# Optimization experiments

Measured on AMD Instinct MI355X. Metric: run time of the kernel, lower is better.

Reference implementation:

```python
import jax, jax.numpy as jnp
import numpy as np

N_HEADS = 12


def _sink_window_visible(S, num_sink_tokens, window_size):
    # visible[i, j] = (j <= i) and (j < num_sink or j >= i - window + 1)
    i = jnp.arange(S)[:, None]
    j = jnp.arange(S)[None, :]
    return (j <= i) & ((j < num_sink_tokens) | (j >= i - window_size + 1))


def setup_inputs() -> dict:
    key = jax.random.key(0)
    k1, k2, k3 = jax.random.split(key, 3)
    B, S, D = 1, 4096, 768
    hidden_states = jax.random.normal(k1, (B, S, D), dtype=jnp.float32)
    w_attn = jax.random.normal(k2, (D, 3 * D), dtype=jnp.float32) * 0.02
    b_attn = jnp.zeros((3 * D,), dtype=jnp.float32)
    w_proj = jax.random.normal(k3, (D, D), dtype=jnp.float32) * 0.02
    b_proj = jnp.zeros((D,), dtype=jnp.float32)
    return {
        "hidden_states": hidden_states,
        "w_attn": w_attn,
        "b_attn": b_attn,
        "w_proj": w_proj,
        "b_proj": b_proj,
        "num_sink_tokens": 4,
        "window_size": 256,
    }


def reference(hidden_states, w_attn, b_attn, w_proj, b_proj, num_sink_tokens, window_size):
    B, S, D = hidden_states.shape
    H = N_HEADS
    hd = D // H
    # GPT-2 fused qkv projection (Conv1D): x @ W + b
    qkv = hidden_states @ w_attn + b_attn  # [B, S, 3D]
    q, k, v = jnp.split(qkv, 3, axis=-1)
    q = q.reshape(B, S, H, hd).transpose(0, 2, 1, 3)  # [B, H, S, hd]
    k = k.reshape(B, S, H, hd).transpose(0, 2, 1, 3)
    v = v.reshape(B, S, H, hd).transpose(0, 2, 1, 3)
    scale = 1.0 / jnp.sqrt(jnp.asarray(hd, dtype=q.dtype))
    scores = jnp.einsum("bhqd,bhkd->bhqk", q, k) * scale  # [B, H, S, S]
    visible = _sink_window_visible(S, num_sink_tokens, window_size)  # [S, S]
    neg = jnp.finfo(scores.dtype).min
    scores = jnp.where(visible[None, None, :, :], scores, neg)
    attn = jax.nn.softmax(scores, axis=-1)
    ctx = jnp.einsum("bhqk,bhkd->bhqd", attn, v)  # [B, H, S, hd]
    ctx = ctx.transpose(0, 2, 1, 3).reshape(B, S, D)
    return ctx @ w_proj + b_proj
```

## Files before the change

### kernel.cpp

```cpp
#include <hip/hip_runtime.h>
#include <hip/hip_bf16.h>
#include <stdint.h>

typedef short bf16x8 __attribute__((ext_vector_type(8)));
typedef unsigned short u16x8 __attribute__((ext_vector_type(8)));
typedef float f32x4 __attribute__((ext_vector_type(4)));

__device__ inline unsigned short f2bf(float f) {
    union { float f; uint32_t u; } v; v.f = f;
    uint32_t lsb = (v.u >> 16) & 1u;
    v.u += 0x7fffu + lsb;
    return (unsigned short)(v.u >> 16);
}

__device__ inline uint32_t cvt_pk_bf16(float lo, float hi) {
    uint32_t r;
    asm("v_cvt_pk_bf16_f32 %0, %1, %2" : "=v"(r) : "v"(lo), "v"(hi));
    return r;
}

__device__ inline void gload16(const unsigned short* g, unsigned short* l) {
    __builtin_amdgcn_global_load_lds(
        (const __attribute__((address_space(1))) unsigned int*)g,
        (__attribute__((address_space(3))) unsigned int*)l, 16, 0, 0);
}

__global__ __launch_bounds__(256) void prep(const float* __restrict__ x,
                                            const float* __restrict__ wa,
                                            const float* __restrict__ wp,
                                            unsigned short* __restrict__ xbf,
                                            unsigned short* __restrict__ waT,
                                            unsigned short* __restrict__ wpT) {
    __shared__ float tile[64][65];
    const int t = threadIdx.x;
    const int id = blockIdx.x;
    if (id < 1536) {
        const int i = id * 256 + t;
        const float4* p = (const float4*)x + (size_t)i * 2;
        float4 a = p[0], b = p[1];
        u16x8 o;
        o[0] = f2bf(a.x); o[1] = f2bf(a.y); o[2] = f2bf(a.z); o[3] = f2bf(a.w);
        o[4] = f2bf(b.x); o[5] = f2bf(b.y); o[6] = f2bf(b.z); o[7] = f2bf(b.w);
        *((u16x8*)xbf + i) = o;
        return;
    }
    const float* in; unsigned short* out; int R, C, bx, by;
    if (id < 1968) { int k = id - 1536; in = wa; out = waT; R = 768; C = 2304; bx = k % 36; by = k / 36; }
    else           { int k = id - 1968; in = wp; out = wpT; R = 768; C = 768;  bx = k % 12; by = k / 12; }
    const int r0 = by * 64, c0 = bx * 64;
    {
        int r = t >> 2, cs = t & 3;
        #pragma unroll
        for (int i = 0; i < 4; ++i) {
            int c = (cs * 4 + i) * 4;
            float4 v = *(const float4*)(in + (size_t)(r0 + r) * C + c0 + c);
            tile[r][c] = v.x; tile[r][c + 1] = v.y; tile[r][c + 2] = v.z; tile[r][c + 3] = v.w;
        }
    }
    __syncthreads();
    {
        int c = t >> 2, rs = t & 3;
        #pragma unroll
        for (int i = 0; i < 2; ++i) {
            u16x8 o;
            #pragma unroll
            for (int e = 0; e < 8; ++e) o[e] = f2bf(tile[rs * 16 + i * 8 + e][c]);
            *(u16x8*)(out + (size_t)(c0 + c) * R + r0 + rs * 16 + i * 8) = o;
        }
    }
}

template <int OUT_BF16, int WRITE_VT>
__global__ __launch_bounds__(256) void gemm_bf16(const unsigned short* __restrict__ A,
                                                 const unsigned short* __restrict__ BT,
                                                 const float* __restrict__ bias,
                                                 void* __restrict__ Cout,
                                                 unsigned short* __restrict__ vTout,
                                                 int M, int N, int K) {
    __shared__ unsigned short As[2][128 * 64];
    __shared__ unsigned short Bs[2][128 * 64];
    const int tid = threadIdx.x;
    const int lane = tid & 63;
    const int w = tid >> 6;
    const int wr = w >> 1, wc = w & 1;
    const int row0 = blockIdx.y * 128, col0 = blockIdx.x * 128;

    const int srow = lane >> 3;
    const int sseg = (lane & 7) ^ srow;

    const int nt = K >> 6;

    f32x4 acc[4][4] = {};

#define STAGE(buf, k0)                                                                     \
    {                                                                                      \
        _Pragma("unroll")                                                                  \
        for (int i = 0; i < 4; ++i) {                                                      \
            const int ch = w * 4 + i;                                                      \
            const int r = ch * 8 + srow;                                                   \
            gload16(A + (size_t)(row0 + r) * K + (k0) + sseg * 8, &As[buf][ch * 512]);     \
            gload16(BT + (size_t)(col0 + r) * K + (k0) + sseg * 8, &Bs[buf][ch * 512]);    \
        }                                                                                  \
    }

    STAGE(0, 0);
    int cur = 0;
    for (int t = 0; t < nt; ++t) {
        __syncthreads();
        if (t + 1 < nt) {
            if (cur) STAGE(0, (t + 1) << 6) else STAGE(1, (t + 1) << 6);
        }
        const unsigned short* as = As[cur];
        const unsigned short* bs = Bs[cur];
        const int c0s = ((0 + (lane >> 4)) ^ (lane & 7)) << 3;
        const int c1s = ((4 + (lane >> 4)) ^ (lane & 7)) << 3;
        bf16x8 af[2][4], bfr[2][4];
        #pragma unroll
        for (int m = 0; m < 4; ++m) {
            const int ra = (wr * 64 + m * 16 + (lane & 15)) * 64;
            const int rb = (wc * 64 + m * 16 + (lane & 15)) * 64;
            af[0][m]  = *(const bf16x8*)(as + ra + c0s);
            af[1][m]  = *(const bf16x8*)(as + ra + c1s);
            bfr[0][m] = *(const bf16x8*)(bs + rb + c0s);
            bfr[1][m] = *(const bf16x8*)(bs + rb + c1s);
        }
        #pragma unroll
        for (int ks = 0; ks < 2; ++ks)
            #pragma unroll
            for (int m = 0; m < 4; ++m)
                #pragma unroll
                for (int n = 0; n < 4; ++n)
                    acc[m][n] = __builtin_amdgcn_mfma_f32_16x16x32_bf16(af[ks][m], bfr[ks][n], acc[m][n], 0, 0, 0);
        cur ^= 1;
    }
#undef STAGE

    if (WRITE_VT && col0 >= 1536) {
        #pragma unroll
        for (int m = 0; m < 4; ++m) {
            int row = row0 + wr * 64 + m * 16 + (lane >> 4) * 4;
            #pragma unroll
            for (int n = 0; n < 4; ++n) {
                int col = col0 + wc * 64 + n * 16 + (lane & 15);
                float bb = bias[col];
                uint2 st;
                st.x = cvt_pk_bf16(acc[m][n][0] + bb, acc[m][n][1] + bb);
                st.y = cvt_pk_bf16(acc[m][n][2] + bb, acc[m][n][3] + bb);
                *(uint2*)(vTout + (size_t)(col - 1536) * 4096 + row) = st;
            }
        }
        return;
    }

    #pragma unroll
    for (int m = 0; m < 4; ++m) {
        int row = row0 + wr * 64 + m * 16 + (lane >> 4) * 4;
        #pragma unroll
        for (int n = 0; n < 4; ++n) {
            int col = col0 + wc * 64 + n * 16 + (lane & 15);
            float bb = bias[col];
            #pragma unroll
            for (int r = 0; r < 4; ++r) {
                float v = acc[m][n][r] + bb;
                if (OUT_BF16)
                    ((unsigned short*)Cout)[(size_t)(row + r) * N + col] = f2bf(v);
                else
                    ((float*)Cout)[(size_t)(row + r) * N + col] = v;
            }
        }
    }
}

__global__ __launch_bounds__(256) void attn_mfma(const unsigned short* __restrict__ qkv,
                                                 const unsigned short* __restrict__ vT,
                                                 unsigned short* __restrict__ ctx,
                                                 const int* __restrict__ pnsink,
                                                 const int* __restrict__ pwin) {
    __shared__ unsigned short Ks0[80 * 64];
    __shared__ unsigned short Vs0[64 * 64 + 2 * 64 * 8];
    __shared__ unsigned short Ks1[64 * 64];
    __shared__ unsigned short Vs1[64 * 64];
    const int tid = threadIdx.x, lane = tid & 63, w = tid >> 6;
    const int q = lane & 15, g = lane >> 4;
    const int h = blockIdx.y;
    const int bx = ((blockIdx.x & 7) << 3) | (blockIdx.x >> 3);
    const int i0 = bx << 6;
    const int nsink = *pnsink, wsize = *pwin;
    const int D3 = 2304;
    const int iq = i0 + 16 * w + q;
    const float SC = 0.18033688011112042f;

    const int sseg = (lane & 7) ^ (lane >> 3);

    const unsigned short* qrow = qkv + (size_t)iq * D3 + h * 64 + g * 8;
    const bf16x8 aq0 = *(const bf16x8*)(qrow);
    const bf16x8 aq1 = *(const bf16x8*)(qrow + 32);

    float m_run = -1e30f, l_run = 0.f;
    f32x4 octx[4] = {};

    int wlo = i0 - wsize + 1; if (wlo < 0) wlo = 0;
    const int t_lo = (wlo >> 6) << 6;
    const bool ext = (t_lo > 0);
    const int ntiles = ((i0 - t_lo) >> 6) + 1;

    const int sl01 = q + ((g & 1) << 5);
    const int sl23 = sl01 + 16;
    const int x7 = q & 7;
    const int ck0 = ((0 + g) ^ x7) << 3;
    const int ck1 = ((4 + g) ^ x7) << 3;

#define ASTAGE(KSB, VSB, kb)                                                           \
    {                                                                                  \
        _Pragma("unroll")                                                              \
        for (int i = 0; i < 2; ++i) {                                                  \
            const int ch = w * 2 + i;                                                  \
            const int r = ch * 8 + (lane >> 3);                                        \
            gload16(qkv + (size_t)((kb) + r) * D3 + 768 + h * 64 + sseg * 8,           \
                    (KSB) + ch * 512);                                                 \
            gload16(vT + ((size_t)h * 64 + r) * 4096 + (kb) + sseg * 8,                \
                    (VSB) + ch * 512);                                                 \
        }                                                                              \
    }

    ASTAGE(Ks0, Vs0, t_lo);
    if (ext) {
        if (w == 0)      gload16(qkv + (size_t)(lane >> 3) * D3 + 768 + h * 64 + sseg * 8, Ks0 + 4096);
        else if (w == 1) gload16(qkv + (size_t)(8 + (lane >> 3)) * D3 + 768 + h * 64 + sseg * 8, Ks0 + 4096 + 512);
        else if (w == 2) gload16(vT + ((size_t)h * 64 + lane) * 4096, Vs0 + 4096);
        else             gload16(vT + ((size_t)h * 64 + lane) * 4096 + 8, Vs0 + 4096 + 1024);
    }

    for (int tt = 0; tt < ntiles; ++tt) {
        __syncthreads();
        if (tt + 1 < ntiles) {
            const int kbn = t_lo + ((tt + 1) << 6);
            if (tt & 1) ASTAGE(Ks0, Vs0, kbn) else ASTAGE(Ks1, Vs1, kbn);
        }
        const int kb = t_lo + (tt << 6);
        const unsigned short* ks_ = (tt & 1) ? Ks1 : Ks0;
        const unsigned short* vs_ = (tt & 1) ? Vs1 : Vs0;
        const bool extt = ext && (tt == 0);
        const int NB = extt ? 5 : 4;

        f32x4 sacc[5] = {};
        __builtin_amdgcn_s_setprio(1);
        #pragma unroll
        for (int nb = 0; nb < 5; ++nb) {
            if (nb < NB) {
                const int rr = (nb * 16 + q) * 64;
                bf16x8 k0 = *(const bf16x8*)(ks_ + rr + ck0);
                bf16x8 k1 = *(const bf16x8*)(ks_ + rr + ck1);
                sacc[nb] = __builtin_amdgcn_mfma_f32_16x16x32_bf16(k0, aq0, sacc[nb], 0, 0, 0);
                sacc[nb] = __builtin_amdgcn_mfma_f32_16x16x32_bf16(k1, aq1, sacc[nb], 0, 0, 0);
            }
        }
        __builtin_amdgcn_s_setprio(0);

        float vmax = -1e30f;
        #pragma unroll
        for (int nb = 0; nb < 5; ++nb)
            if (nb < NB)
                #pragma unroll
                for (int r = 0; r < 4; ++r) {
                    const int slot = nb * 16 + g * 4 + r;
                    const int j = (slot >= 64) ? (slot - 64) : kb + slot;
                    const bool vis = (j <= iq) && ((j < nsink) || (j > iq - wsize));
                    sacc[nb][r] = vis ? sacc[nb][r] * SC : -1e30f;
                    vmax = fmaxf(vmax, sacc[nb][r]);
                }
        vmax = fmaxf(vmax, __shfl_xor(vmax, 16));
        vmax = fmaxf(vmax, __shfl_xor(vmax, 32));

        const bool upd = !__all(vmax <= m_run + 8.f);
        if (upd) {
            const float mn = fmaxf(m_run, vmax);
            const float alpha = __builtin_amdgcn_exp2f(m_run - mn);
            l_run *= alpha;
            #pragma unroll
            for (int nb = 0; nb < 4; ++nb)
                #pragma unroll
                for (int r = 0; r < 4; ++r) octx[nb][r] *= alpha;
            m_run = mn;
        }
        float p[5][4];
        float lsum = 0.f;
        #pragma unroll
        for (int nb = 0; nb < 5; ++nb)
            if (nb < NB)
                #pragma unroll
                for (int r = 0; r < 4; ++r) {
                    const float pv = __builtin_amdgcn_exp2f(sacc[nb][r] - m_run);
                    p[nb][r] = pv;
                    lsum += pv;
                }
        lsum += __shfl_xor(lsum, 16);
        lsum += __shfl_xor(lsum, 32);
        l_run += lsum;

        uint32_t c01[5][2];
        #pragma unroll
        for (int nb = 0; nb < 5; ++nb)
            if (nb < NB) {
                c01[nb][0] = cvt_pk_bf16(p[nb][0], p[nb][1]);
                c01[nb][1] = cvt_pk_bf16(p[nb][2], p[nb][3]);
            }

        __builtin_amdgcn_s_setprio(1);
        #pragma unroll
        for (int ks = 0; ks < 2; ++ks) {
            uint32_t f00 = (uint32_t)__shfl((int)c01[2 * ks + 0][0], sl01);
            uint32_t f01 = (uint32_t)__shfl((int)c01[2 * ks + 1][0], sl01);
            uint32_t f10 = (uint32_t)__shfl((int)c01[2 * ks + 0][1], sl01);
            uint32_t f11 = (uint32_t)__shfl((int)c01[2 * ks + 1][1], sl01);
            uint32_t f20 = (uint32_t)__shfl((int)c01[2 * ks + 0][0], sl23);
            uint32_t f21 = (uint32_t)__shfl((int)c01[2 * ks + 1][0], sl23);
            uint32_t f30 = (uint32_t)__shfl((int)c01[2 * ks + 0][1], sl23);
            uint32_t f31 = (uint32_t)__shfl((int)c01[2 * ks + 1][1], sl23);
            union { uint32_t u[4]; bf16x8 v; } pa;
            pa.u[0] = (g >> 1) ? f01 : f00;
            pa.u[1] = (g >> 1) ? f11 : f10;
            pa.u[2] = (g >> 1) ? f21 : f20;
            pa.u[3] = (g >> 1) ? f31 : f30;
            const int cv = ((ks * 4 + g) ^ x7) << 3;
            #pragma unroll
            for (int nb = 0; nb < 4; ++nb) {
                bf16x8 bv = *(const bf16x8*)(vs_ + (nb * 16 + q) * 64 + cv);
                octx[nb] = __builtin_amdgcn_mfma_f32_16x16x32_bf16(bv, pa.v, octx[nb], 0, 0, 0);
            }
        }
        if (extt) {
            uint32_t e0 = (uint32_t)__shfl((int)c01[4][0], sl01);
            uint32_t e1 = (uint32_t)__shfl((int)c01[4][1], sl01);
            uint32_t e2 = (uint32_t)__shfl((int)c01[4][0], sl23);
            uint32_t e3 = (uint32_t)__shfl((int)c01[4][1], sl23);
            union { uint32_t u[4]; bf16x8 v; } pa;
            const bool lo = (g < 2);
            pa.u[0] = lo ? e0 : 0u;
            pa.u[1] = lo ? e1 : 0u;
            pa.u[2] = lo ? e2 : 0u;
            pa.u[3] = lo ? e3 : 0u;
            const unsigned short* vb = vs_ + 4096 + ((g & 1) << 10);
            #pragma unroll
            for (int nb = 0; nb < 4; ++nb) {
                bf16x8 bv = *(const bf16x8*)(vb + (nb * 16 + q) * 8);
                octx[nb] = __builtin_amdgcn_mfma_f32_16x16x32_bf16(bv, pa.v, octx[nb], 0, 0, 0);
            }
        }
        __builtin_amdgcn_s_setprio(0);
    }
#undef ASTAGE

    const float inv = (l_run > 0.f) ? 1.f / l_run : 0.f;
    unsigned short* crow = ctx + (size_t)iq * 768 + h * 64 + g * 4;
    #pragma unroll
    for (int nb = 0; nb < 4; ++nb) {
        uint2 st;
        st.x = cvt_pk_bf16(octx[nb][0] * inv, octx[nb][1] * inv);
        st.y = cvt_pk_bf16(octx[nb][2] * inv, octx[nb][3] * inv);
        *(uint2*)(crow + nb * 16) = st;
    }
}

extern "C" void kernel_launch(void* const* d_in, const int* in_sizes, int n_in,
                              void* d_out, int out_size, void* d_ws, size_t ws_size,
                              hipStream_t stream) {
    const float* x      = (const float*)d_in[0];
    const float* w_attn = (const float*)d_in[1];
    const float* b_attn = (const float*)d_in[2];
    const float* w_proj = (const float*)d_in[3];
    const float* b_proj = (const float*)d_in[4];
    const int*   pnsink = (const int*)d_in[5];
    const int*   pwin   = (const int*)d_in[6];
    float* out = (float*)d_out;

    const int D = 768, S = 4096, N1 = 3 * D;

    unsigned short* xbf   = (unsigned short*)d_ws;
    unsigned short* waT   = xbf + (size_t)S * D;
    unsigned short* wpT   = waT + (size_t)N1 * D;
    unsigned short* qkvbf = wpT + (size_t)D * D;
    unsigned short* ctxbf = qkvbf + (size_t)S * N1;
    unsigned short* vTbf  = ctxbf + (size_t)S * D;

    prep<<<2112, 256, 0, stream>>>(x, w_attn, w_proj, xbf, waT, wpT);

    {
        dim3 g(N1 / 128, S / 128);
        gemm_bf16<1, 1><<<g, 256, 0, stream>>>(xbf, waT, b_attn, qkvbf, vTbf, S, N1, D);
    }
    {
        dim3 g(S / 64, 12);
        attn_mfma<<<g, 256, 0, stream>>>(qkvbf, vTbf, ctxbf, pnsink, pwin);
    }
    {
        dim3 g(D / 128, S / 128);
        gemm_bf16<0, 0><<<g, 256, 0, stream>>>(ctxbf, wpT, b_proj, out, nullptr, S, D, D);
    }
}
```

Before: 71.07 us.

## Use 256x256-tile 8-phase pipelined MFMA GEMM for QKV projection

Adds a new GEMM kernel for the QKV projection. It uses 256x256 output tiles, 512 threads and double-buffered LDS halves. The loop is split into phases that interleave global-to-LDS loads with MFMA clusters, using barriers and s_setprio to overlap memory and compute. The goal is more operand reuse per load and better latency hiding. The trade-off is a much smaller grid (144 blocks) and heavy LDS use, which may leave many CUs idle.

```diff
diff --git a/kernel.cpp b/kernel.cpp
--- a/kernel.cpp
+++ b/kernel.cpp
@@ -71,6 +71,134 @@
 }
 
 template <int OUT_BF16, int WRITE_VT>
+__global__ __launch_bounds__(512, 2) void gemm256_8ph(
+    const unsigned short* __restrict__ A, const unsigned short* __restrict__ BT,
+    const float* __restrict__ bias, void* __restrict__ Cout,
+    unsigned short* __restrict__ vTout, int M, int N, int K) {
+    __shared__ unsigned short LA[2][2][128 * 64];
+    __shared__ unsigned short LB[2][2][128 * 64];
+    const int tid = threadIdx.x, lane = tid & 63, w = tid >> 6;
+    const int wr = w >> 2, wc = w & 3;
+    const int row0 = blockIdx.y * 256, col0 = blockIdx.x * 256;
+    const int g = lane >> 4, arow = lane & 15;
+    const int sseg = (lane & 7) ^ (lane >> 3);
+    const int ck0 = ((0 + g) ^ (lane & 7)) << 3;
+    const int ck1 = ((4 + g) ^ (lane & 7)) << 3;
+    const int ha = wr;
+    const int hb = wc >> 1;
+    const int bc0 = (wc & 1) * 64;
+    const int NT = K >> 6;
+
+    f32x4 acc[8][4] = {};
+
+#define STG_A(buf, half, t)                                                              \
+    { _Pragma("unroll")                                                                  \
+      for (int i = 0; i < 2; ++i) {                                                      \
+          const int r = i * 64 + w * 8 + (lane >> 3);                                    \
+          gload16(A + (size_t)(row0 + (half) * 128 + r) * K + ((t) << 6) + sseg * 8,     \
+                  &LA[buf][half][i * 4096 + w * 512]);                                   \
+      } }
+#define STG_B(buf, half, t)                                                              \
+    { _Pragma("unroll")                                                                  \
+      for (int i = 0; i < 2; ++i) {                                                      \
+          const int r = i * 64 + w * 8 + (lane >> 3);                                    \
+          gload16(BT + (size_t)(col0 + (half) * 128 + r) * K + ((t) << 6) + sseg * 8,    \
+                  &LB[buf][half][i * 4096 + w * 512]);                                   \
+      } }
+#define MMCL(AF, BF, MLO)                                                                \
+    { _Pragma("unroll")                                                                  \
+      for (int m = 0; m < 4; ++m)                                                        \
+          _Pragma("unroll")                                                              \
+          for (int n = 0; n < 4; ++n)                                                    \
+              acc[(MLO) + m][n] = __builtin_amdgcn_mfma_f32_16x16x32_bf16(               \
+                  AF[(MLO) + m], BF[n], acc[(MLO) + m][n], 0, 0, 0); }
+
+    STG_A(0, 0, 0); STG_A(0, 1, 0); STG_B(0, 0, 0); STG_B(0, 1, 0);
+    STG_A(1, 0, 1); STG_A(1, 1, 1);
+    asm volatile("s_waitcnt vmcnt(4)" ::: "memory");
+    __builtin_amdgcn_s_barrier();
+
+    for (int t = 0; t < NT; ++t) {
+        const int buf = t & 1, nbuf = buf ^ 1;
+        const unsigned short* Ab = LA[buf][ha];
+        const unsigned short* Bb = LB[buf][hb];
+        bf16x8 a0[8], a1[8], b0[4], b1[4];
+        #pragma unroll
+        for (int m = 0; m < 8; ++m) a0[m] = *(const bf16x8*)(Ab + (m * 16 + arow) * 64 + ck0);
+        #pragma unroll
+        for (int n = 0; n < 4; ++n) b0[n] = *(const bf16x8*)(Bb + (bc0 + n * 16 + arow) * 64 + ck0);
+        if (t + 1 < NT) STG_B(nbuf, 0, t + 1);
+        __builtin_amdgcn_s_barrier();
+        __builtin_amdgcn_s_setprio(1);
+        MMCL(a0, b0, 0);
+        __builtin_amdgcn_s_setprio(0);
+        __builtin_amdgcn_s_barrier();
+        #pragma unroll
+        for (int m = 0; m < 8; ++m) a1[m] = *(const bf16x8*)(Ab + (m * 16 + arow) * 64 + ck1);
+        #pragma unroll
+        for (int n = 0; n < 4; ++n) b1[n] = *(const bf16x8*)(Bb + (bc0 + n * 16 + arow) * 64 + ck1);
+        if (t + 1 < NT) STG_B(nbuf, 1, t + 1);
+        __builtin_amdgcn_s_barrier();
+        __builtin_amdgcn_s_setprio(1);
+        MMCL(a0, b0, 4);
+        __builtin_amdgcn_s_setprio(0);
+        asm volatile("s_waitcnt lgkmcnt(0)" ::: "memory");
+        __builtin_amdgcn_s_barrier();
+        if (t + 2 < NT) STG_A(buf, 0, t + 2);
+        __builtin_amdgcn_s_barrier();
+        __builtin_amdgcn_s_setprio(1);
+        MMCL(a1, b1, 0);
+        __builtin_amdgcn_s_setprio(0);
+        __builtin_amdgcn_s_barrier();
+        if (t + 2 < NT) STG_A(buf, 1, t + 2);
+        __builtin_amdgcn_s_barrier();
+        __builtin_amdgcn_s_setprio(1);
+        MMCL(a1, b1, 4);
+        __builtin_amdgcn_s_setprio(0);
+        if (t < NT - 2)       asm volatile("s_waitcnt vmcnt(4)" ::: "memory");
+        else if (t == NT - 2) asm volatile("s_waitcnt vmcnt(0)" ::: "memory");
+        __builtin_amdgcn_s_barrier();
+    }
+#undef STG_A
+#undef STG_B
+#undef MMCL
+
+    if (WRITE_VT && col0 >= 1536) {
+        #pragma unroll
+        for (int m = 0; m < 8; ++m) {
+            int row = row0 + wr * 128 + m * 16 + g * 4;
+            #pragma unroll
+            for (int n = 0; n < 4; ++n) {
+                int col = col0 + wc * 64 + n * 16 + arow;
+                float bb = bias[col];
+                uint2 st;
+                st.x = cvt_pk_bf16(acc[m][n][0] + bb, acc[m][n][1] + bb);
+                st.y = cvt_pk_bf16(acc[m][n][2] + bb, acc[m][n][3] + bb);
+                *(uint2*)(vTout + (size_t)(col - 1536) * 4096 + row) = st;
+            }
+        }
+        return;
+    }
+    #pragma unroll
+    for (int m = 0; m < 8; ++m) {
+        int row = row0 + wr * 128 + m * 16 + g * 4;
+        #pragma unroll
+        for (int n = 0; n < 4; ++n) {
+            int col = col0 + wc * 64 + n * 16 + arow;
+            float bb = bias[col];
+            #pragma unroll
+            for (int r = 0; r < 4; ++r) {
+                float v = acc[m][n][r] + bb;
+                if (OUT_BF16)
+                    ((unsigned short*)Cout)[(size_t)(row + r) * N + col] = f2bf(v);
+                else
+                    ((float*)Cout)[(size_t)(row + r) * N + col] = v;
+            }
+        }
+    }
+}
+
+template <int OUT_BF16, int WRITE_VT>
 __global__ __launch_bounds__(256) void gemm_bf16(const unsigned short* __restrict__ A,
                                                  const unsigned short* __restrict__ BT,
                                                  const float* __restrict__ bias,
@@ -386,8 +514,8 @@
     prep<<<2112, 256, 0, stream>>>(x, w_attn, w_proj, xbf, waT, wpT);
 
     {
-        dim3 g(N1 / 128, S / 128);
-        gemm_bf16<1, 1><<<g, 256, 0, stream>>>(xbf, waT, b_attn, qkvbf, vTbf, S, N1, D);
+        dim3 g(N1 / 256, S / 256);
+        gemm256_8ph<1, 1><<<g, 512, 0, stream>>>(xbf, waT, b_attn, qkvbf, vTbf, S, N1, D);
     }
     {
         dim3 g(S / 64, 12);
```

New measurement: 73.08 us. 1.03x slower.
